# Performance work log

Hardware: AMD Instinct MI355X
Metric: run time of the kernel (lower is better)

Reference implementation:

```python
import jax, jax.numpy as jnp
import numpy as np

IN_F = 128
OUT_F = 128
N_LAYER = 2
DEPTH = 9                       # tree depth -> levels 0..DEPTH-1
N_TREES = 128
TREE_SIZE = 2 ** DEPTH - 1      # 511 nodes per complete binary tree
N = N_TREES * TREE_SIZE         # 65408 total nodes
E = N_TREES * (TREE_SIZE - 1)   # 65280 parent->child edges


def _build_forest():
    """Complete binary trees in heap layout; leaves get order 0, root order DEPTH-1."""
    k = np.arange(TREE_SIZE)
    depth = np.floor(np.log2(k + 1)).astype(np.int32)
    order_tree = (DEPTH - 1) - depth                      # per-node level within a tree
    node_order = np.tile(order_tree, N_TREES).astype(np.int32)
    internal = k[k < 2 ** (DEPTH - 1) - 1]                # internal nodes have 2 children
    par = np.repeat(internal, 2)
    chi = np.empty_like(par)
    chi[0::2] = 2 * internal + 1
    chi[1::2] = 2 * internal + 2
    eorder_tree = order_tree[par]
    offs = (np.arange(N_TREES) * TREE_SIZE)[:, None]
    parents = (par[None, :] + offs).reshape(-1)
    children = (chi[None, :] + offs).reshape(-1)
    adjacency = np.stack([parents, children], axis=1).astype(np.int32)
    edge_order = np.tile(eorder_tree, N_TREES).astype(np.int32)
    return node_order, adjacency, edge_order


def setup_inputs() -> dict:
    key = jax.random.key(0)
    ks = jax.random.split(key, 8)
    node_order, adjacency, edge_order = _build_forest()
    s = 0.05
    return {
        "features": jax.random.normal(ks[0], (N, IN_F), jnp.float32),
        "W_iou": jax.random.normal(ks[1], (N_LAYER, 3 * OUT_F, IN_F), jnp.float32) * s,
        "b_iou": jax.random.normal(ks[2], (N_LAYER, 3 * OUT_F), jnp.float32) * s,
        "U_iou": jax.random.normal(ks[3], (N_LAYER, 3 * OUT_F, OUT_F), jnp.float32) * s,
        "W_f": jax.random.normal(ks[4], (N_LAYER, OUT_F, IN_F), jnp.float32) * s,
        "b_f": jax.random.normal(ks[5], (N_LAYER, OUT_F), jnp.float32) * s,
        "U_f": jax.random.normal(ks[6], (N_LAYER, OUT_F, OUT_F), jnp.float32) * s,
        "node_order": jnp.asarray(node_order),
        "adjacency_list": jnp.asarray(adjacency),
        "edge_order": jnp.asarray(edge_order),
        "treesizes": jnp.full((N_TREES,), TREE_SIZE, jnp.int32),
        "n_levels": DEPTH,
    }


def reference(features, W_iou, b_iou, U_iou, W_f, b_f, U_f,
              node_order, adjacency_list, edge_order, treesizes, n_levels):
    n_nodes = features.shape[0]
    parent = adjacency_list[:, 0]
    child = adjacency_list[:, 1]
    n_trees = treesizes.shape[0]
    tree_size = n_nodes // n_trees
    # root of each (equal-sized) tree = argmax of node_order within its segment
    root_idx = (jnp.argmax(node_order.reshape(n_trees, tree_size), axis=1)
                + jnp.arange(n_trees) * tree_size)

    def run_layer(Wi, bi, Ui, Wf, bf, Uf):
        Wx_iou = features @ Wi.T + bi              # [N, 3H], level-independent
        Wfx = features[parent] @ Wf.T + bf         # [E, H], per-edge forget input
        H = Wi.shape[0] // 3

        def step(carry, lvl):
            h, c = carry
            em = (edge_order == lvl).astype(features.dtype)[:, None]   # [E,1]
            ch = h[child]                                              # gather child h
            cc = c[child]
            h_sum = jax.ops.segment_sum(ch * em, parent, num_segments=n_nodes)
            iou = Wx_iou + h_sum @ Ui.T
            i_, o_, u_ = jnp.split(iou, 3, axis=1)
            i_ = jax.nn.sigmoid(i_)
            o_ = jax.nn.sigmoid(o_)
            u_ = jnp.tanh(u_)
            f = jax.nn.sigmoid(Wfx + ch @ Uf.T)                        # [E,H]
            c_sum = jax.ops.segment_sum(f * cc * em, parent, num_segments=n_nodes)
            c_new = i_ * u_ + c_sum
            h_new = o_ * jnp.tanh(c_new)
            nm = (node_order == lvl)[:, None]
            return (jnp.where(nm, h_new, h), jnp.where(nm, c_new, c)), None

        init = (jnp.zeros((n_nodes, H), features.dtype),
                jnp.zeros((n_nodes, H), features.dtype))
        (h, c), _ = jax.lax.scan(step, init, jnp.arange(n_levels))
        return h[root_idx], c[root_idx]

    f_h, f_c = jax.vmap(run_layer)(W_iou, b_iou, U_iou, W_f, b_f, U_f)
    return f_h, f_c
```

## Files before the change

### kernel.cpp

```cpp
#include <hip/hip_runtime.h>
#include <hip/hip_bf16.h>


#define TS 511
#define NT 128

typedef __attribute__((ext_vector_type(8))) short short8;
typedef __attribute__((ext_vector_type(4))) float floatx4;

#define MFMA_B16 __builtin_amdgcn_mfma_f32_16x16x32_bf16

__device__ __forceinline__ unsigned short f2b(float f) {
    return __builtin_bit_cast(unsigned short, __float2bfloat16(f));
}
__device__ __forceinline__ float b2f_u(unsigned short u) {
    unsigned v = (unsigned)u << 16;
    return __builtin_bit_cast(float, v);
}
__device__ __forceinline__ float rcp_(float x) { return __builtin_amdgcn_rcpf(x); }
__device__ __forceinline__ float sig_(float x) { return rcp_(1.0f + __expf(-x)); }
__device__ __forceinline__ float tanh_(float x) {
    float a = fabsf(x);
    float t = __expf(-2.0f * a);
    return copysignf((1.0f - t) * rcp_(1.0f + t), x);
}

__global__ void pack_b(const float* __restrict__ Wiou, const float* __restrict__ biou,
                       const float* __restrict__ Uiou, const float* __restrict__ Wf,
                       const float* __restrict__ bfv, const float* __restrict__ Uf,
                       unsigned short* __restrict__ BgU, unsigned short* __restrict__ BgX,
                       float* __restrict__ bp5) {
    int tid = blockIdx.x * 256 + threadIdx.x;
    if (tid < 1280) {
        int l = tid / 640, r = tid % 640, g = r >> 7, o = r & 127;
        bp5[tid] = (g < 3) ? biou[l * 384 + r] : bfv[l * 128 + o];
    }
    if (tid < 131072) {
        int l = tid >> 16, r = tid & 65535, col = r >> 7, kp = r & 127;
        float v = (col < 384) ? Uiou[(l * 384 + col) * 128 + kp]
                              : Uf[(l * 128 + (col - 384)) * 128 + kp];
        BgU[((size_t)(l * 512 + col)) * 128 + kp] = f2b(v);
    } else if (tid < 262144) {
        int e2 = tid - 131072;
        int l = e2 >> 16, r = e2 & 65535, col = r >> 7, kp = r & 127;
        float v = (col < 384) ? Wiou[(l * 384 + col) * 128 + kp]
                              : Wf[(l * 128 + (col - 384)) * 128 + kp];
        BgX[((size_t)(l * 512 + col)) * 128 + kp] = f2b(v);
    }
}

__global__ __launch_bounds__(512) void forest(
        const float* __restrict__ feat, const unsigned short* __restrict__ BgU,
        const unsigned short* __restrict__ BgX, const float* __restrict__ bp5,
        float* __restrict__ out) {
    __shared__ unsigned short S[69632];
    const int HC0 = 26112, LFH0 = 52224, LFC0 = 60928;

    const int tid = threadIdx.x;
    const int l = blockIdx.x >> 7, tree = blockIdx.x & 127;
    const int lane = tid & 63, w = tid >> 6;
    const int quad = lane >> 4, l15 = lane & 15;
    const int o = w * 16 + l15;
    const float* xb = feat + (size_t)tree * TS * 128;
    const unsigned short* BU = BgU + (size_t)l * 512 * 128;
    const unsigned short* BX = BgX + (size_t)l * 512 * 128;

    short8 bU[4][4], bX[4][4];
#pragma unroll
    for (int g = 0; g < 4; g++) {
        const size_t cb = (size_t)(g * 128 + o) * 128;
#pragma unroll
        for (int kbl = 0; kbl < 4; kbl++) {
            bU[g][kbl] = *(const short8*)(BU + cb + kbl * 32 + quad * 8);
            bX[g][kbl] = *(const short8*)(BX + cb + kbl * 32 + quad * 8);
        }
    }
    float bb[5];
#pragma unroll
    for (int g = 0; g < 5; g++) bb[g] = bp5[l * 640 + g * 128 + o];

    auto loadx8 = [&](int heap, int kbl) -> short8 {
        const float* p = xb + (size_t)heap * 128 + kbl * 32 + quad * 8;
        float4 u0 = *(const float4*)p;
        float4 u1 = *(const float4*)(p + 4);
        short8 r;
        r[0] = (short)f2b(u0.x); r[1] = (short)f2b(u0.y);
        r[2] = (short)f2b(u0.z); r[3] = (short)f2b(u0.w);
        r[4] = (short)f2b(u1.x); r[5] = (short)f2b(u1.y);
        r[6] = (short)f2b(u1.z); r[7] = (short)f2b(u1.w);
        return r;
    };

    short8 lxs[2][4];
    short8 axd[4];

    auto leafload = [&](int mt) {
#pragma unroll
        for (int lm = 0; lm < 2; lm++)
#pragma unroll
            for (int kbl = 0; kbl < 4; kbl++)
                lxs[lm][kbl] = loadx8(255 + mt * 32 + lm * 16 + l15, kbl);
    };
    auto leafcomp = [&](int buf) {
        const int LB = LFH0 + buf * 4352;
        const int LCB = LFC0 + buf * 4352;
#pragma unroll
        for (int lm = 0; lm < 2; lm++) {
            floatx4 a0 = (floatx4){0.f, 0.f, 0.f, 0.f};
            floatx4 a1 = a0, a2 = a0;
#pragma unroll
            for (int kbl = 0; kbl < 4; kbl++) {
                a0 = MFMA_B16(lxs[lm][kbl], bX[0][kbl], a0, 0, 0, 0);
                a1 = MFMA_B16(lxs[lm][kbl], bX[1][kbl], a1, 0, 0, 0);
                a2 = MFMA_B16(lxs[lm][kbl], bX[2][kbl], a2, 0, 0, 0);
            }
#pragma unroll
            for (int r = 0; r < 4; r++) {
                float iv = sig_(a0[r] + bb[0]);
                float ov = sig_(a1[r] + bb[1]);
                float uv = tanh_(a2[r] + bb[2]);
                float cn = iv * uv;
                float hn = ov * tanh_(cn);
                int lr = lm * 16 + quad * 4 + r;
                S[LB + lr * 136 + o] = f2b(hn);
                S[LCB + lr * 136 + o] = f2b(cn);
            }
        }
    };
    auto d7comp = [&](int mt, int buf) {
        const int LB = LFH0 + buf * 4352;
        const int LCB = LFC0 + buf * 4352;
        floatx4 ac0 = (floatx4){0.f, 0.f, 0.f, 0.f};
        floatx4 ac1 = ac0, ac2 = ac0, ac3 = ac0, ac4 = ac0;
#pragma unroll
        for (int kbl = 0; kbl < 4; kbl++) {
            short8 h0 = *(const short8*)&S[LB + (2 * l15) * 136 + kbl * 32 + quad * 8];
            short8 h1 = *(const short8*)&S[LB + (2 * l15 + 1) * 136 + kbl * 32 + quad * 8];
            short8 ax = axd[kbl];
            ac0 = MFMA_B16(ax, bX[0][kbl], ac0, 0, 0, 0);
            ac0 = MFMA_B16(h0, bU[0][kbl], ac0, 0, 0, 0);
            ac0 = MFMA_B16(h1, bU[0][kbl], ac0, 0, 0, 0);
            ac1 = MFMA_B16(ax, bX[1][kbl], ac1, 0, 0, 0);
            ac1 = MFMA_B16(h0, bU[1][kbl], ac1, 0, 0, 0);
            ac1 = MFMA_B16(h1, bU[1][kbl], ac1, 0, 0, 0);
            ac2 = MFMA_B16(ax, bX[2][kbl], ac2, 0, 0, 0);
            ac2 = MFMA_B16(h0, bU[2][kbl], ac2, 0, 0, 0);
            ac2 = MFMA_B16(h1, bU[2][kbl], ac2, 0, 0, 0);
            ac3 = MFMA_B16(ax, bX[3][kbl], ac3, 0, 0, 0);
            ac3 = MFMA_B16(h0, bU[3][kbl], ac3, 0, 0, 0);
            ac4 = MFMA_B16(ax, bX[3][kbl], ac4, 0, 0, 0);
            ac4 = MFMA_B16(h1, bU[3][kbl], ac4, 0, 0, 0);
        }
#pragma unroll
        for (int r = 0; r < 4; r++) {
            int rE = quad * 4 + r;
            float iv = sig_(ac0[r] + bb[0]);
            float ov = sig_(ac1[r] + bb[1]);
            float uv = tanh_(ac2[r] + bb[2]);
            float f0 = sig_(ac3[r] + bb[3]);
            float f1 = sig_(ac4[r] + bb[4]);
            float c0 = b2f_u(S[LCB + (2 * rE) * 136 + o]);
            float c1 = b2f_u(S[LCB + (2 * rE + 1) * 136 + o]);
            float cn = iv * uv + f0 * c0 + f1 * c1;
            float hn = ov * tanh_(cn);
            int sr = mt * 16 + rE;
            S[sr * 136 + o] = f2b(hn);
            S[HC0 + sr * 136 + o] = f2b(cn);
        }
    };

    leafload(0);
    leafcomp(0);
    __syncthreads();
#pragma unroll 1
    for (int mt = 0; mt < 8; mt++) {
#pragma unroll
        for (int kbl = 0; kbl < 4; kbl++) axd[kbl] = loadx8(127 + mt * 16 + l15, kbl);
        if (mt < 7) leafload(mt + 1);
        d7comp(mt, mt & 1);
        if (mt < 7) leafcomp((mt + 1) & 1);
        __syncthreads();
    }

#pragma unroll
    for (int dd = 6; dd >= 0; dd--) {
        const int nd = 1 << dd;
        const int selfB = (dd == 6) ? 128 : 64 - 2 * nd;
        const int chB = (dd == 6) ? 0 : ((dd == 5) ? 128 : 64 - 4 * nd);
        const int mts = (nd + 15) >> 4;
#pragma unroll
        for (int mt = 0; mt < mts; mt++) {
            const int rloc = (l15 < nd) ? (mt * 16 + l15) : (nd - 1);
            const int heap = nd - 1 + rloc;
            floatx4 ac0 = (floatx4){0.f, 0.f, 0.f, 0.f};
            floatx4 ac1 = ac0, ac2 = ac0, ac3 = ac0, ac4 = ac0;
#pragma unroll
            for (int kbl = 0; kbl < 4; kbl++) {
                short8 ax = loadx8(heap, kbl);
                short8 h0 = *(const short8*)&S[(chB + 2 * rloc) * 136 + kbl * 32 + quad * 8];
                short8 h1 = *(const short8*)&S[(chB + 2 * rloc + 1) * 136 + kbl * 32 + quad * 8];
                ac0 = MFMA_B16(ax, bX[0][kbl], ac0, 0, 0, 0);
                ac0 = MFMA_B16(h0, bU[0][kbl], ac0, 0, 0, 0);
                ac0 = MFMA_B16(h1, bU[0][kbl], ac0, 0, 0, 0);
                ac1 = MFMA_B16(ax, bX[1][kbl], ac1, 0, 0, 0);
                ac1 = MFMA_B16(h0, bU[1][kbl], ac1, 0, 0, 0);
                ac1 = MFMA_B16(h1, bU[1][kbl], ac1, 0, 0, 0);
                ac2 = MFMA_B16(ax, bX[2][kbl], ac2, 0, 0, 0);
                ac2 = MFMA_B16(h0, bU[2][kbl], ac2, 0, 0, 0);
                ac2 = MFMA_B16(h1, bU[2][kbl], ac2, 0, 0, 0);
                ac3 = MFMA_B16(ax, bX[3][kbl], ac3, 0, 0, 0);
                ac3 = MFMA_B16(h0, bU[3][kbl], ac3, 0, 0, 0);
                ac4 = MFMA_B16(ax, bX[3][kbl], ac4, 0, 0, 0);
                ac4 = MFMA_B16(h1, bU[3][kbl], ac4, 0, 0, 0);
            }
#pragma unroll
            for (int r = 0; r < 4; r++) {
                int rE = mt * 16 + quad * 4 + r;
                if (rE < nd) {
                    float iv = sig_(ac0[r] + bb[0]);
                    float ov = sig_(ac1[r] + bb[1]);
                    float uv = tanh_(ac2[r] + bb[2]);
                    float f0 = sig_(ac3[r] + bb[3]);
                    float f1 = sig_(ac4[r] + bb[4]);
                    float c0 = b2f_u(S[HC0 + (chB + 2 * rE) * 136 + o]);
                    float c1 = b2f_u(S[HC0 + (chB + 2 * rE + 1) * 136 + o]);
                    float cn = iv * uv + f0 * c0 + f1 * c1;
                    float hn = ov * tanh_(cn);
                    S[(selfB + rE) * 136 + o] = f2b(hn);
                    S[HC0 + (selfB + rE) * 136 + o] = f2b(cn);
                    if (dd == 0) {
                        out[((size_t)l * 128 + tree) * 128 + o] = hn;
                        out[32768 + ((size_t)l * 128 + tree) * 128 + o] = cn;
                    }
                }
            }
        }
        __syncthreads();
    }
}

extern "C" void kernel_launch(void* const* d_in, const int* in_sizes, int n_in,
                              void* d_out, int out_size, void* d_ws, size_t ws_size,
                              hipStream_t stream) {
    const float* feat = (const float*)d_in[0];
    const float* Wiou = (const float*)d_in[1];
    const float* biou = (const float*)d_in[2];
    const float* Uiou = (const float*)d_in[3];
    const float* Wf   = (const float*)d_in[4];
    const float* bfv  = (const float*)d_in[5];
    const float* Uf   = (const float*)d_in[6];
    float* out = (float*)d_out;

    unsigned short* BgU = (unsigned short*)d_ws;
    unsigned short* BgX = BgU + (size_t)131072;
    float* bp5 = (float*)(BgX + (size_t)131072);

    pack_b<<<1024, 256, 0, stream>>>(Wiou, biou, Uiou, Wf, bfv, Uf, BgU, BgX, bp5);
    forest<<<256, 512, 0, stream>>>(feat, BgU, BgX, bp5, out);
}
```

Baseline: 179.4 us.

## Pre-convert features to bf16 in pack kernel and restructure forest tiles

```diff
diff --git a/kernel.cpp b/kernel.cpp
--- a/kernel.cpp
+++ b/kernel.cpp
@@ -4,11 +4,18 @@
 
 #define TS 511
 #define NT 128
+#define NN (NT * TS)
 
 typedef __attribute__((ext_vector_type(8))) short short8;
 typedef __attribute__((ext_vector_type(4))) float floatx4;
 
 #define MFMA_B16 __builtin_amdgcn_mfma_f32_16x16x32_bf16
+
+#define BARLDS() do { \
+    asm volatile("s_waitcnt lgkmcnt(0)" ::: "memory"); \
+    __builtin_amdgcn_s_barrier(); \
+    asm volatile("" ::: "memory"); \
+} while (0)
 
 __device__ __forceinline__ unsigned short f2b(float f) {
     return __builtin_bit_cast(unsigned short, __float2bfloat16(f));
@@ -28,8 +35,9 @@
 __global__ void pack_b(const float* __restrict__ Wiou, const float* __restrict__ biou,
                        const float* __restrict__ Uiou, const float* __restrict__ Wf,
                        const float* __restrict__ bfv, const float* __restrict__ Uf,
+                       const float* __restrict__ feat,
                        unsigned short* __restrict__ BgU, unsigned short* __restrict__ BgX,
-                       float* __restrict__ bp5) {
+                       float* __restrict__ bp5, unsigned short* __restrict__ xb) {
     int tid = blockIdx.x * 256 + threadIdx.x;
     if (tid < 1280) {
         int l = tid / 640, r = tid % 640, g = r >> 7, o = r & 127;
@@ -46,22 +54,33 @@
         float v = (col < 384) ? Wiou[(l * 384 + col) * 128 + kp]
                               : Wf[(l * 128 + (col - 384)) * 128 + kp];
         BgX[((size_t)(l * 512 + col)) * 128 + kp] = f2b(v);
-    }
-}
-
-__global__ __launch_bounds__(512) void forest(
-        const float* __restrict__ feat, const unsigned short* __restrict__ BgU,
+    } else {
+        int e = tid - 262144;
+        size_t base = (size_t)e * 8;
+        float4 v0 = *(const float4*)(feat + base);
+        float4 v1 = *(const float4*)(feat + base + 4);
+        short8 r;
+        r[0] = (short)f2b(v0.x); r[1] = (short)f2b(v0.y);
+        r[2] = (short)f2b(v0.z); r[3] = (short)f2b(v0.w);
+        r[4] = (short)f2b(v1.x); r[5] = (short)f2b(v1.y);
+        r[6] = (short)f2b(v1.z); r[7] = (short)f2b(v1.w);
+        *(short8*)(xb + base) = r;
+    }
+}
+
+__global__ __launch_bounds__(512, 2) void forest(
+        const unsigned short* __restrict__ xb16, const unsigned short* __restrict__ BgU,
         const unsigned short* __restrict__ BgX, const float* __restrict__ bp5,
         float* __restrict__ out) {
-    __shared__ unsigned short S[69632];
-    const int HC0 = 26112, LFH0 = 52224, LFC0 = 60928;
+    __shared__ __align__(16) unsigned short S[69632];
+    const int HC0 = 26112;
 
     const int tid = threadIdx.x;
     const int l = blockIdx.x >> 7, tree = blockIdx.x & 127;
     const int lane = tid & 63, w = tid >> 6;
     const int quad = lane >> 4, l15 = lane & 15;
     const int o = w * 16 + l15;
-    const float* xb = feat + (size_t)tree * TS * 128;
+    const unsigned short* xb = xb16 + (size_t)tree * TS * 128;
     const unsigned short* BU = BgU + (size_t)l * 512 * 128;
     const unsigned short* BX = BgX + (size_t)l * 512 * 128;
 
@@ -79,107 +98,99 @@
 #pragma unroll
     for (int g = 0; g < 5; g++) bb[g] = bp5[l * 640 + g * 128 + o];
 
-    auto loadx8 = [&](int heap, int kbl) -> short8 {
-        const float* p = xb + (size_t)heap * 128 + kbl * 32 + quad * 8;
-        float4 u0 = *(const float4*)p;
-        float4 u1 = *(const float4*)(p + 4);
-        short8 r;
-        r[0] = (short)f2b(u0.x); r[1] = (short)f2b(u0.y);
-        r[2] = (short)f2b(u0.z); r[3] = (short)f2b(u0.w);
-        r[4] = (short)f2b(u1.x); r[5] = (short)f2b(u1.y);
-        r[6] = (short)f2b(u1.z); r[7] = (short)f2b(u1.w);
-        return r;
+    auto ldx = [&](int heap, int kbl) -> short8 {
+        return *(const short8*)(xb + (size_t)heap * 128 + kbl * 32 + quad * 8);
     };
 
-    short8 lxs[2][4];
-    short8 axd[4];
-
-    auto leafload = [&](int mt) {
-#pragma unroll
-        for (int lm = 0; lm < 2; lm++)
-#pragma unroll
-            for (int kbl = 0; kbl < 4; kbl++)
-                lxs[lm][kbl] = loadx8(255 + mt * 32 + lm * 16 + l15, kbl);
+    auto ltile = [&](int heapA, int selfH, int selfC) {
+        floatx4 ai = (floatx4){0.f, 0.f, 0.f, 0.f};
+        floatx4 ao = ai, au = ai;
+#pragma unroll
+        for (int kbl = 0; kbl < 4; kbl++) {
+            short8 ax = ldx(heapA, kbl);
+            ai = MFMA_B16(ax, bX[0][kbl], ai, 0, 0, 0);
+            ao = MFMA_B16(ax, bX[1][kbl], ao, 0, 0, 0);
+            au = MFMA_B16(ax, bX[2][kbl], au, 0, 0, 0);
+        }
+#pragma unroll
+        for (int r = 0; r < 4; r++) {
+            int idx = quad * 4 + r;
+            float iv = sig_(ai[r] + bb[0]);
+            float ov = sig_(ao[r] + bb[1]);
+            float uv = tanh_(au[r] + bb[2]);
+            float cn = iv * uv;
+            float hn = ov * tanh_(cn);
+            S[(selfH + idx) * 136 + o] = f2b(hn);
+            S[HC0 + (selfC + idx) * 136 + o] = f2b(cn);
+        }
     };
-    auto leafcomp = [&](int buf) {
-        const int LB = LFH0 + buf * 4352;
-        const int LCB = LFC0 + buf * 4352;
-#pragma unroll
-        for (int lm = 0; lm < 2; lm++) {
-            floatx4 a0 = (floatx4){0.f, 0.f, 0.f, 0.f};
-            floatx4 a1 = a0, a2 = a0;
-#pragma unroll
-            for (int kbl = 0; kbl < 4; kbl++) {
-                a0 = MFMA_B16(lxs[lm][kbl], bX[0][kbl], a0, 0, 0, 0);
-                a1 = MFMA_B16(lxs[lm][kbl], bX[1][kbl], a1, 0, 0, 0);
-                a2 = MFMA_B16(lxs[lm][kbl], bX[2][kbl], a2, 0, 0, 0);
+
+    auto itile = [&](int heapA, int chAh, int selfRB, int chRBc,
+                     int nValid, bool isRoot) {
+        floatx4 ai = (floatx4){0.f, 0.f, 0.f, 0.f};
+        floatx4 ao = ai, au = ai, awx = ai, af0 = ai, af1 = ai;
+#pragma unroll
+        for (int kbl = 0; kbl < 4; kbl++) {
+            short8 h0 = *(const short8*)&S[chAh * 136 + kbl * 32 + quad * 8];
+            short8 h1 = *(const short8*)&S[(chAh + 1) * 136 + kbl * 32 + quad * 8];
+            short8 ax = ldx(heapA, kbl);
+            ai = MFMA_B16(h0, bU[0][kbl], ai, 0, 0, 0);
+            ai = MFMA_B16(h1, bU[0][kbl], ai, 0, 0, 0);
+            ao = MFMA_B16(h0, bU[1][kbl], ao, 0, 0, 0);
+            ao = MFMA_B16(h1, bU[1][kbl], ao, 0, 0, 0);
+            au = MFMA_B16(h0, bU[2][kbl], au, 0, 0, 0);
+            au = MFMA_B16(h1, bU[2][kbl], au, 0, 0, 0);
+            af0 = MFMA_B16(h0, bU[3][kbl], af0, 0, 0, 0);
+            af1 = MFMA_B16(h1, bU[3][kbl], af1, 0, 0, 0);
+            ai = MFMA_B16(ax, bX[0][kbl], ai, 0, 0, 0);
+            ao = MFMA_B16(ax, bX[1][kbl], ao, 0, 0, 0);
+            au = MFMA_B16(ax, bX[2][kbl], au, 0, 0, 0);
+            awx = MFMA_B16(ax, bX[3][kbl], awx, 0, 0, 0);
+        }
+#pragma unroll
+        for (int r = 0; r < 4; r++) {
+            int idx = quad * 4 + r;
+            if (idx < nValid) {
+                float iv = sig_(ai[r] + bb[0]);
+                float ov = sig_(ao[r] + bb[1]);
+                float uv = tanh_(au[r] + bb[2]);
+                float f0 = sig_(awx[r] + af0[r] + bb[3]);
+                float f1 = sig_(awx[r] + af1[r] + bb[4]);
+                float c0 = b2f_u(S[HC0 + (chRBc + 2 * idx) * 136 + o]);
+                float c1 = b2f_u(S[HC0 + (chRBc + 2 * idx + 1) * 136 + o]);
+                float cn = iv * uv + f0 * c0 + f1 * c1;
+                float hn = ov * tanh_(cn);
+                S[(selfRB + idx) * 136 + o] = f2b(hn);
+                S[HC0 + (selfRB + idx) * 136 + o] = f2b(cn);
+                if (isRoot) {
+                    out[((size_t)l * 128 + tree) * 128 + o] = hn;
+                    out[32768 + ((size_t)l * 128 + tree) * 128 + o] = cn;
+                }
             }
-#pragma unroll
-            for (int r = 0; r < 4; r++) {
-                float iv = sig_(a0[r] + bb[0]);
-                float ov = sig_(a1[r] + bb[1]);
-                float uv = tanh_(a2[r] + bb[2]);
-                float cn = iv * uv;
-                float hn = ov * tanh_(cn);
-                int lr = lm * 16 + quad * 4 + r;
-                S[LB + lr * 136 + o] = f2b(hn);
-                S[LCB + lr * 136 + o] = f2b(cn);
-            }
         }
     };
-    auto d7comp = [&](int mt, int buf) {
-        const int LB = LFH0 + buf * 4352;
-        const int LCB = LFC0 + buf * 4352;
-        floatx4 ac0 = (floatx4){0.f, 0.f, 0.f, 0.f};
-        floatx4 ac1 = ac0, ac2 = ac0, ac3 = ac0, ac4 = ac0;
-#pragma unroll
-        for (int kbl = 0; kbl < 4; kbl++) {
-            short8 h0 = *(const short8*)&S[LB + (2 * l15) * 136 + kbl * 32 + quad * 8];
-            short8 h1 = *(const short8*)&S[LB + (2 * l15 + 1) * 136 + kbl * 32 + quad * 8];
-            short8 ax = axd[kbl];
-            ac0 = MFMA_B16(ax, bX[0][kbl], ac0, 0, 0, 0);
-            ac0 = MFMA_B16(h0, bU[0][kbl], ac0, 0, 0, 0);
-            ac0 = MFMA_B16(h1, bU[0][kbl], ac0, 0, 0, 0);
-            ac1 = MFMA_B16(ax, bX[1][kbl], ac1, 0, 0, 0);
-            ac1 = MFMA_B16(h0, bU[1][kbl], ac1, 0, 0, 0);
-            ac1 = MFMA_B16(h1, bU[1][kbl], ac1, 0, 0, 0);
-            ac2 = MFMA_B16(ax, bX[2][kbl], ac2, 0, 0, 0);
-            ac2 = MFMA_B16(h0, bU[2][kbl], ac2, 0, 0, 0);
-            ac2 = MFMA_B16(h1, bU[2][kbl], ac2, 0, 0, 0);
-            ac3 = MFMA_B16(ax, bX[3][kbl], ac3, 0, 0, 0);
-            ac3 = MFMA_B16(h0, bU[3][kbl], ac3, 0, 0, 0);
-            ac4 = MFMA_B16(ax, bX[3][kbl], ac4, 0, 0, 0);
-            ac4 = MFMA_B16(h1, bU[3][kbl], ac4, 0, 0, 0);
-        }
-#pragma unroll
-        for (int r = 0; r < 4; r++) {
-            int rE = quad * 4 + r;
-            float iv = sig_(ac0[r] + bb[0]);
-            float ov = sig_(ac1[r] + bb[1]);
-            float uv = tanh_(ac2[r] + bb[2]);
-            float f0 = sig_(ac3[r] + bb[3]);
-            float f1 = sig_(ac4[r] + bb[4]);
-            float c0 = b2f_u(S[LCB + (2 * rE) * 136 + o]);
-            float c1 = b2f_u(S[LCB + (2 * rE + 1) * 136 + o]);
-            float cn = iv * uv + f0 * c0 + f1 * c1;
-            float hn = ov * tanh_(cn);
-            int sr = mt * 16 + rE;
-            S[sr * 136 + o] = f2b(hn);
-            S[HC0 + sr * 136 + o] = f2b(cn);
-        }
-    };
-
-    leafload(0);
-    leafcomp(0);
-    __syncthreads();
-#pragma unroll 1
-    for (int mt = 0; mt < 8; mt++) {
-#pragma unroll
-        for (int kbl = 0; kbl < 4; kbl++) axd[kbl] = loadx8(127 + mt * 16 + l15, kbl);
-        if (mt < 7) leafload(mt + 1);
-        d7comp(mt, mt & 1);
-        if (mt < 7) leafcomp((mt + 1) & 1);
-        __syncthreads();
+
+#pragma unroll
+    for (int s = 0; s < 2; s++)
+        ltile(255 + s * 16 + l15, 384 + s * 16, 256 + s * 16);
+    BARLDS();
+
+#pragma unroll 2
+    for (int t = 0; t < 8; t++) {
+        if (t < 7) {
+            int b2 = (t + 1) & 1;
+#pragma unroll
+            for (int s = 0; s < 2; s++)
+                ltile(255 + (t + 1) * 32 + s * 16 + l15,
+                      384 + b2 * 32 + s * 16, 256 + b2 * 32 + s * 16);
+        }
+        int b = t & 1;
+        itile(127 + t * 16 + l15,
+              384 + b * 32 + 2 * l15,
+              t * 16,
+              256 + b * 32,
+              16, false);
+        BARLDS();
     }
 
 #pragma unroll
@@ -190,52 +201,17 @@
         const int mts = (nd + 15) >> 4;
 #pragma unroll
         for (int mt = 0; mt < mts; mt++) {
-            const int rloc = (l15 < nd) ? (mt * 16 + l15) : (nd - 1);
-            const int heap = nd - 1 + rloc;
-            floatx4 ac0 = (floatx4){0.f, 0.f, 0.f, 0.f};
-            floatx4 ac1 = ac0, ac2 = ac0, ac3 = ac0, ac4 = ac0;
-#pragma unroll
-            for (int kbl = 0; kbl < 4; kbl++) {
-                short8 ax = loadx8(heap, kbl);
-                short8 h0 = *(const short8*)&S[(chB + 2 * rloc) * 136 + kbl * 32 + quad * 8];
-                short8 h1 = *(const short8*)&S[(chB + 2 * rloc + 1) * 136 + kbl * 32 + quad * 8];
-                ac0 = MFMA_B16(ax, bX[0][kbl], ac0, 0, 0, 0);
-                ac0 = MFMA_B16(h0, bU[0][kbl], ac0, 0, 0, 0);
-                ac0 = MFMA_B16(h1, bU[0][kbl], ac0, 0, 0, 0);
-                ac1 = MFMA_B16(ax, bX[1][kbl], ac1, 0, 0, 0);
-                ac1 = MFMA_B16(h0, bU[1][kbl], ac1, 0, 0, 0);
-                ac1 = MFMA_B16(h1, bU[1][kbl], ac1, 0, 0, 0);
-                ac2 = MFMA_B16(ax, bX[2][kbl], ac2, 0, 0, 0);
-                ac2 = MFMA_B16(h0, bU[2][kbl], ac2, 0, 0, 0);
-                ac2 = MFMA_B16(h1, bU[2][kbl], ac2, 0, 0, 0);
-                ac3 = MFMA_B16(ax, bX[3][kbl], ac3, 0, 0, 0);
-                ac3 = MFMA_B16(h0, bU[3][kbl], ac3, 0, 0, 0);
-                ac4 = MFMA_B16(ax, bX[3][kbl], ac4, 0, 0, 0);
-                ac4 = MFMA_B16(h1, bU[3][kbl], ac4, 0, 0, 0);
-            }
-#pragma unroll
-            for (int r = 0; r < 4; r++) {
-                int rE = mt * 16 + quad * 4 + r;
-                if (rE < nd) {
-                    float iv = sig_(ac0[r] + bb[0]);
-                    float ov = sig_(ac1[r] + bb[1]);
-                    float uv = tanh_(ac2[r] + bb[2]);
-                    float f0 = sig_(ac3[r] + bb[3]);
-                    float f1 = sig_(ac4[r] + bb[4]);
-                    float c0 = b2f_u(S[HC0 + (chB + 2 * rE) * 136 + o]);
-                    float c1 = b2f_u(S[HC0 + (chB + 2 * rE + 1) * 136 + o]);
-                    float cn = iv * uv + f0 * c0 + f1 * c1;
-                    float hn = ov * tanh_(cn);
-                    S[(selfB + rE) * 136 + o] = f2b(hn);
-                    S[HC0 + (selfB + rE) * 136 + o] = f2b(cn);
-                    if (dd == 0) {
-                        out[((size_t)l * 128 + tree) * 128 + o] = hn;
-                        out[32768 + ((size_t)l * 128 + tree) * 128 + o] = cn;
-                    }
-                }
-            }
-        }
-        __syncthreads();
+            int rl = mt * 16 + l15;
+            if (rl > nd - 1) rl = nd - 1;
+            int nv = nd - mt * 16;
+            if (nv > 16) nv = 16;
+            itile(nd - 1 + rl,
+                  chB + 2 * rl,
+                  selfB + mt * 16,
+                  chB + 2 * mt * 16,
+                  nv, dd == 0);
+        }
+        BARLDS();
     }
 }
 
@@ -253,8 +229,10 @@
 
     unsigned short* BgU = (unsigned short*)d_ws;
     unsigned short* BgX = BgU + (size_t)131072;
-    float* bp5 = (float*)(BgX + (size_t)131072);
-
-    pack_b<<<1024, 256, 0, stream>>>(Wiou, biou, Uiou, Wf, bfv, Uf, BgU, BgX, bp5);
-    forest<<<256, 512, 0, stream>>>(feat, BgU, BgX, bp5, out);
-}
+    unsigned short* xb16 = BgX + (size_t)131072;
+    float* bp5 = (float*)(xb16 + (size_t)NN * 128);
+
+    pack_b<<<5112, 256, 0, stream>>>(Wiou, biou, Uiou, Wf, bfv, Uf, feat,
+                                     BgU, BgX, bp5, xb16);
+    forest<<<256, 512, 0, stream>>>(xb16, BgU, BgX, bp5, out);
+}
```

New measurement: 157.6 us. 1.14x faster.
